# Performance work log

Hardware: AMD Instinct MI355X
Metric: run time of the kernel (lower is better)

The kernel has to match this reference:

```python
import jax, jax.numpy as jnp
import numpy as np

N, E = 50000, 800000
IN_DIM, HID, HEADS, OUT_DIM = 128, 64, 4, 40
NEG_SLOPE = 0.2


def setup_inputs() -> dict:
    key = jax.random.key(0)
    ks = jax.random.split(key, 12)
    x = jax.random.normal(ks[0], (N, IN_DIM), dtype=jnp.float32)
    edge_index = jax.random.randint(ks[1], (2, E), 0, N, dtype=jnp.int64)
    timesteps = jax.random.randint(ks[2], (N,), 0, 100, dtype=jnp.int64)
    s = 1.0 / np.sqrt(IN_DIM)
    W_proj = jax.random.uniform(ks[3], (IN_DIM, HID), jnp.float32, -s, s)
    b_proj = jnp.zeros((HID,), jnp.float32)
    time_emb = jax.random.normal(ks[4], (100, HID), dtype=jnp.float32)
    sg = 1.0 / np.sqrt(HID)
    W_gat = jax.random.uniform(ks[5], (HID, HEADS * HID), jnp.float32, -sg, sg)
    att_src = jax.random.uniform(ks[6], (HEADS, HID), jnp.float32, -sg, sg)
    att_dst = jax.random.uniform(ks[7], (HEADS, HID), jnp.float32, -sg, sg)
    b_gat = jnp.zeros((HEADS * HID,), jnp.float32)
    sc = 1.0 / np.sqrt(HEADS * HID)
    W_cls = jax.random.uniform(ks[8], (HEADS * HID, OUT_DIM), jnp.float32, -sc, sc)
    b_cls = jnp.zeros((OUT_DIM,), jnp.float32)
    return {"x": x, "edge_index": edge_index, "timesteps": timesteps,
            "W_proj": W_proj, "b_proj": b_proj, "time_emb": time_emb,
            "W_gat": W_gat, "att_src": att_src, "att_dst": att_dst, "b_gat": b_gat,
            "W_cls": W_cls, "b_cls": b_cls}


def reference(x, edge_index, timesteps, W_proj, b_proj, time_emb,
              W_gat, att_src, att_dst, b_gat, W_cls, b_cls):
    n = x.shape[0]
    # feature projection + ReLU + time embedding
    h0 = jax.nn.relu(x @ W_proj + b_proj) + time_emb[timesteps]  # [N, HID]
    # --- GATConv (PyG semantics, add_self_loops=True, concat heads) ---
    h = (h0 @ W_gat).reshape(n, HEADS, HID)              # [N, H, C]
    a_src = jnp.einsum('nhc,hc->nh', h, att_src)         # [N, H]
    a_dst = jnp.einsum('nhc,hc->nh', h, att_dst)
    loops = jnp.arange(n, dtype=edge_index.dtype)
    src = jnp.concatenate([edge_index[0], loops])        # [E+N]
    dst = jnp.concatenate([edge_index[1], loops])
    e = jax.nn.leaky_relu(a_src[src] + a_dst[dst], NEG_SLOPE)  # [E+N, H]
    # segment softmax over incoming edges per destination node
    m = jax.ops.segment_max(e, dst, num_segments=n)      # [N, H]
    p = jnp.exp(e - m[dst])
    denom = jax.ops.segment_sum(p, dst, num_segments=n)  # [N, H]
    alpha = p / (denom[dst] + 1e-16)                     # [E+N, H]
    msg = alpha[:, :, None] * h[src]                     # [E+N, H, C]
    agg = jax.ops.segment_sum(msg, dst, num_segments=n)  # [N, H, C]
    gat_out = agg.reshape(n, HEADS * HID) + b_gat
    # ReLU + (dropout is identity in eval) + classifier
    return jax.nn.relu(gat_out) @ W_cls + b_cls          # [N, OUT_DIM]
```

## Files before the change

### kernel.cpp

```cpp
#include <hip/hip_runtime.h>
#include <hip/hip_fp16.h>

#define IN_DIM 128
#define HID 64
#define HEADS 4
#define OUT_DIM 40
#define CAP 64
#define NEG 0.2f
#define PA_EPB 4096
#define BKT_SH 9
#define BKT_CAP 10240
#define GPAD 264

__device__ __forceinline__ float lrelu(float v) { return v > 0.f ? v : NEG * v; }

union HU { float2 f2; __half2 h2[2]; };
union HU2 { float4 f4; __half2 h2[4]; };

typedef _Float16 h2v __attribute__((ext_vector_type(2)));
union DU { float4 f4; h2v h[4]; };

typedef _Float16 f16x8 __attribute__((ext_vector_type(8)));
typedef float f32x4 __attribute__((ext_vector_type(4)));
union FU { float4 f4; f16x8 v; };

__device__ __forceinline__ float4 unpack_h4(float2 bits) {
    HU u; u.f2 = bits;
    float2 lo = __half22float2(u.h2[0]);
    float2 hi = __half22float2(u.h2[1]);
    return make_float4(lo.x, lo.y, hi.x, hi.y);
}

__global__ __launch_bounds__(256) void partA_kernel(
    const int* __restrict__ ei, int E, int nbkt, int paBlocks,
    int* __restrict__ cnt, unsigned int* __restrict__ ebuf,
    const float* __restrict__ Wg, const float* __restrict__ attS,
    const float* __restrict__ attD, const float* __restrict__ Wc,
    float* __restrict__ aSf, float* __restrict__ aDf,
    __half* __restrict__ WgT, __half* __restrict__ WcTg)
{
    if (blockIdx.x >= paBlocks) {
        int gid = (blockIdx.x - paBlocks) * 256 + threadIdx.x;
        if (gid < 256) {
            int k = gid >> 2, hd = gid & 3;
            const float* wr = Wg + k * 256 + hd * 64;
            const float* as = attS + hd * 64;
            const float* ad = attD + hd * 64;
            float ss = 0.f, dd = 0.f;
            for (int c = 0; c < 64; ++c) { float w = wr[c]; ss += w * as[c]; dd += w * ad[c]; }
            aSf[k * 4 + hd] = ss;
            aDf[k * 4 + hd] = dd;
        } else if (gid < 256 + 256 * HID) {
            int i = gid - 256;
            int o = i >> 6, k = i & 63;
            WgT[i] = __float2half(Wg[k * 256 + o]);
        } else if (gid < 256 + 256 * HID + OUT_DIM * 256) {
            int i = gid - 256 - 256 * HID;
            int o = i >> 8, k = i & 255;
            WcTg[i] = __float2half(Wc[k * OUT_DIM + o]);
        }
        return;
    }

    __shared__ int localCnt[128];
    __shared__ int baseArr[128];
    for (int i = threadIdx.x; i < nbkt; i += 256) localCnt[i] = 0;
    __syncthreads();

    const int e0 = blockIdx.x * PA_EPB + threadIdx.x;
    unsigned short l[16];
#pragma unroll
    for (int j = 0; j < 16; ++j) {
        int e = e0 + j * 256;
        if (e < E) {
            int d = ei[E + e];
            l[j] = (unsigned short)atomicAdd(&localCnt[d >> BKT_SH], 1);
        }
    }
    __syncthreads();
    for (int i = threadIdx.x; i < nbkt; i += 256)
        baseArr[i] = atomicAdd(&cnt[i], localCnt[i]);
    __syncthreads();
#pragma unroll
    for (int j = 0; j < 16; ++j) {
        int e = e0 + j * 256;
        if (e < E) {
            int s = ei[e];
            int d = ei[E + e];
            int b = d >> BKT_SH;
            int off = baseArr[b] + (int)l[j];
            if (off < BKT_CAP)
                ebuf[(size_t)b * BKT_CAP + off] =
                    ((unsigned)(d & ((1 << BKT_SH) - 1)) << 16) | (unsigned)s;
        }
    }
}

__global__ __launch_bounds__(256) void partBproj_kernel(
    const unsigned int* __restrict__ ebuf, const int* __restrict__ cnt,
    int* __restrict__ deg, unsigned short* __restrict__ csr, int nbkt,
    const float* __restrict__ x, const float* __restrict__ Wp,
    const float* __restrict__ bp, const float* __restrict__ temb,
    const int* __restrict__ ts, const float* __restrict__ aSf,
    const float* __restrict__ aDf,
    __half* __restrict__ h0h, float* __restrict__ aS, float* __restrict__ aD, int N)
{
    __shared__ __align__(16) char smem[IN_DIM * HID * 2];

    if ((int)blockIdx.x < nbkt) {
        int* cntL = (int*)smem;
        const int b = blockIdx.x;
        for (int i = threadIdx.x; i < 512; i += 256) cntL[i] = 0;
        __syncthreads();

        int cb = cnt[b]; cb = cb < BKT_CAP ? cb : BKT_CAP;
        const unsigned int* eb = ebuf + (size_t)b * BKT_CAP;
        const int d0 = b << BKT_SH;
        for (int i = threadIdx.x; i < cb; i += 256) {
            unsigned v = eb[i];
            int dloc = v >> 16;
            int slot = atomicAdd(&cntL[dloc], 1);
            if (slot < CAP)
                csr[((size_t)(d0 + dloc) << 6) + slot] = (unsigned short)(v & 0xFFFFu);
        }
        __syncthreads();
        for (int i = threadIdx.x; i < 512; i += 256) {
            int d = d0 + i;
            if (d < N) deg[d] = cntL[i];
        }
        return;
    }

    __half* Wl = (__half*)smem;
    for (int i = threadIdx.x * 8; i < IN_DIM * HID; i += 256 * 8) {
        float4 wa = *(const float4*)(Wp + i);
        float4 wb = *(const float4*)(Wp + i + 4);
        HU2 u;
        u.h2[0] = __floats2half2_rn(wa.x, wa.y);
        u.h2[1] = __floats2half2_rn(wa.z, wa.w);
        u.h2[2] = __floats2half2_rn(wb.x, wb.y);
        u.h2[3] = __floats2half2_rn(wb.z, wb.w);
        *(float4*)(Wl + i) = u.f4;
    }
    __syncthreads();

    const int t = threadIdx.x;
    const int lane = t & 63, wq = t >> 6;
    const int cg = lane & 15, ng = lane >> 4;
    const int c0 = cg * 4;
    const int nodeBase = ((int)blockIdx.x - nbkt) * 32 + wq * 8 + ng * 2;

    float4 acc[2];
#pragma unroll
    for (int j = 0; j < 2; ++j) acc[j] = make_float4(0.f, 0.f, 0.f, 0.f);

    for (int k0 = 0; k0 < IN_DIM; k0 += 4) {
        float4 xv[2];
#pragma unroll
        for (int j = 0; j < 2; ++j) {
            int n = nodeBase + j; n = n < N ? n : N - 1;
            xv[j] = *(const float4*)(x + (size_t)n * IN_DIM + k0);
        }
        float4 wv[4];
#pragma unroll
        for (int kk = 0; kk < 4; ++kk)
            wv[kk] = unpack_h4(*(const float2*)(Wl + (k0 + kk) * HID + c0));
#pragma unroll
        for (int j = 0; j < 2; ++j) {
            const float* xs = (const float*)&xv[j];
#pragma unroll
            for (int kk = 0; kk < 4; ++kk) {
                acc[j].x += xs[kk] * wv[kk].x;
                acc[j].y += xs[kk] * wv[kk].y;
                acc[j].z += xs[kk] * wv[kk].z;
                acc[j].w += xs[kk] * wv[kk].w;
            }
        }
    }
    const float4 bb = *(const float4*)(bp + c0);
    float4 s0 = *(const float4*)(aSf + (c0 + 0) * 4);
    float4 s1 = *(const float4*)(aSf + (c0 + 1) * 4);
    float4 s2 = *(const float4*)(aSf + (c0 + 2) * 4);
    float4 s3 = *(const float4*)(aSf + (c0 + 3) * 4);
    float4 d0 = *(const float4*)(aDf + (c0 + 0) * 4);
    float4 d1 = *(const float4*)(aDf + (c0 + 1) * 4);
    float4 d2 = *(const float4*)(aDf + (c0 + 2) * 4);
    float4 d3 = *(const float4*)(aDf + (c0 + 3) * 4);
#pragma unroll
    for (int j = 0; j < 2; ++j) {
        int n = nodeBase + j;
        float4 r = make_float4(0.f, 0.f, 0.f, 0.f);
        if (n < N) {
            int tv = ts[n];
            float4 te = *(const float4*)(temb + (size_t)tv * HID + c0);
            r.x = fmaxf(acc[j].x + bb.x, 0.f) + te.x;
            r.y = fmaxf(acc[j].y + bb.y, 0.f) + te.y;
            r.z = fmaxf(acc[j].z + bb.z, 0.f) + te.z;
            r.w = fmaxf(acc[j].w + bb.w, 0.f) + te.w;
            HU u;
            u.h2[0] = __floats2half2_rn(r.x, r.y);
            u.h2[1] = __floats2half2_rn(r.z, r.w);
            *(float2*)(h0h + (size_t)n * HID + c0) = u.f2;
        }
        float4 pS, pD;
        pS.x = r.x * s0.x + r.y * s1.x + r.z * s2.x + r.w * s3.x;
        pS.y = r.x * s0.y + r.y * s1.y + r.z * s2.y + r.w * s3.y;
        pS.z = r.x * s0.z + r.y * s1.z + r.z * s2.z + r.w * s3.z;
        pS.w = r.x * s0.w + r.y * s1.w + r.z * s2.w + r.w * s3.w;
        pD.x = r.x * d0.x + r.y * d1.x + r.z * d2.x + r.w * d3.x;
        pD.y = r.x * d0.y + r.y * d1.y + r.z * d2.y + r.w * d3.y;
        pD.z = r.x * d0.z + r.y * d1.z + r.z * d2.z + r.w * d3.z;
        pD.w = r.x * d0.w + r.y * d1.w + r.z * d2.w + r.w * d3.w;
#pragma unroll
        for (int off = 8; off > 0; off >>= 1) {
            pS.x += __shfl_down(pS.x, off); pS.y += __shfl_down(pS.y, off);
            pS.z += __shfl_down(pS.z, off); pS.w += __shfl_down(pS.w, off);
            pD.x += __shfl_down(pD.x, off); pD.y += __shfl_down(pD.y, off);
            pD.z += __shfl_down(pD.z, off); pD.w += __shfl_down(pD.w, off);
        }
        if (cg == 0 && n < N) {
            *(float4*)(aS + (size_t)n * 4) = pS;
            *(float4*)(aD + (size_t)n * 4) = pD;
        }
    }
}

__global__ __launch_bounds__(256) void agg_kernel(
    const __half* __restrict__ h0h, const float* __restrict__ aS,
    const float* __restrict__ aD, const int* __restrict__ deg,
    const unsigned short* __restrict__ csr, __half* __restrict__ agg0h, int N)
{
    __shared__ float p_lds[4 * CAP * HEADS];
    __shared__ int   s_lds[4 * CAP];

    const int t = threadIdx.x;
    const int lane = t & 63, wq = t >> 6;
    const int n = blockIdx.x * 4 + wq;
    if (n >= N) return;
    const int hd16 = lane >> 4, li = lane & 15;

    const float adn = aD[n * 4 + hd16];
    const float es = lrelu(aS[n * 4 + hd16] + adn);

    int dn = deg[n]; dn = dn < CAP ? dn : CAP;
    const unsigned short* cs = csr + (size_t)n * CAP;
    float* pL = p_lds + wq * CAP * HEADS;
    int*   sL = s_lds + wq * CAP;

    float m = -1e30f;
    for (int i = li; i < dn; i += 16) {
        int src = cs[i];
        if (hd16 == 0) sL[i] = src << 7;
        float e = lrelu(aS[src * 4 + hd16] + adn);
        pL[i * HEADS + hd16] = e;
        m = fmaxf(m, e);
    }
#pragma unroll
    for (int off = 8; off > 0; off >>= 1)
        m = fmaxf(m, __shfl_xor(m, off));
    m = fmaxf(m, es);
    float mh[4], esh[4];
#pragma unroll
    for (int h = 0; h < 4; ++h) {
        mh[h]  = __shfl(m, h * 16);
        esh[h] = __shfl(es, h * 16);
    }

    float sp = 0.f;
    for (int idx = lane; idx < dn * 4; idx += 64) {
        float p = __expf(pL[idx] - mh[idx & 3]);
        pL[idx] = p;
        sp += p;
    }
#pragma unroll
    for (int off = 4; off < 64; off <<= 1)
        sp += __shfl_xor(sp, off);
    float pselfh[4], invh[4];
#pragma unroll
    for (int h = 0; h < 4; ++h) {
        float sh = __shfl(sp, h);
        pselfh[h] = __expf(esh[h] - mh[h]);
        invh[h] = 1.f / (sh + pselfh[h] + 1e-16f);
    }

    const int half = lane >> 5;
    const int ch2 = lane & 31;
    const char* hb = (const char*)h0h;
    const int laneByte = ch2 << 2;

    float2 acc[4];
    {
        float lo = 0.f, hi = 0.f;
        if (half == 0) {
            __half2 v2 = *(const __half2*)(hb + ((size_t)n << 7) + laneByte);
            float2 f = __half22float2(v2);
            lo = f.x; hi = f.y;
        }
#pragma unroll
        for (int h = 0; h < 4; ++h) {
            acc[h].x = pselfh[h] * lo;
            acc[h].y = pselfh[h] * hi;
        }
    }
    int i = 0;
    for (; i + 8 <= dn; i += 8) {
        int off0 = sL[i + 0 + half];
        int off1 = sL[i + 2 + half];
        int off2 = sL[i + 4 + half];
        int off3 = sL[i + 6 + half];
        __half2 v0 = *(const __half2*)(hb + off0 + laneByte);
        __half2 v1 = *(const __half2*)(hb + off1 + laneByte);
        __half2 v2 = *(const __half2*)(hb + off2 + laneByte);
        __half2 v3 = *(const __half2*)(hb + off3 + laneByte);
        float4 p0 = *(const float4*)(pL + (i + 0 + half) * 4);
        float4 p1 = *(const float4*)(pL + (i + 2 + half) * 4);
        float4 p2 = *(const float4*)(pL + (i + 4 + half) * 4);
        float4 p3 = *(const float4*)(pL + (i + 6 + half) * 4);
        float2 f;
        f = __half22float2(v0);
        acc[0].x += p0.x * f.x; acc[0].y += p0.x * f.y;
        acc[1].x += p0.y * f.x; acc[1].y += p0.y * f.y;
        acc[2].x += p0.z * f.x; acc[2].y += p0.z * f.y;
        acc[3].x += p0.w * f.x; acc[3].y += p0.w * f.y;
        f = __half22float2(v1);
        acc[0].x += p1.x * f.x; acc[0].y += p1.x * f.y;
        acc[1].x += p1.y * f.x; acc[1].y += p1.y * f.y;
        acc[2].x += p1.z * f.x; acc[2].y += p1.z * f.y;
        acc[3].x += p1.w * f.x; acc[3].y += p1.w * f.y;
        f = __half22float2(v2);
        acc[0].x += p2.x * f.x; acc[0].y += p2.x * f.y;
        acc[1].x += p2.y * f.x; acc[1].y += p2.y * f.y;
        acc[2].x += p2.z * f.x; acc[2].y += p2.z * f.y;
        acc[3].x += p2.w * f.x; acc[3].y += p2.w * f.y;
        f = __half22float2(v3);
        acc[0].x += p3.x * f.x; acc[0].y += p3.x * f.y;
        acc[1].x += p3.y * f.x; acc[1].y += p3.y * f.y;
        acc[2].x += p3.z * f.x; acc[2].y += p3.z * f.y;
        acc[3].x += p3.w * f.x; acc[3].y += p3.w * f.y;
    }
    for (; i + 2 <= dn; i += 2) {
        int off0 = sL[i + half];
        __half2 v0 = *(const __half2*)(hb + off0 + laneByte);
        float4 p0 = *(const float4*)(pL + (i + half) * 4);
        float2 f = __half22float2(v0);
        acc[0].x += p0.x * f.x; acc[0].y += p0.x * f.y;
        acc[1].x += p0.y * f.x; acc[1].y += p0.y * f.y;
        acc[2].x += p0.z * f.x; acc[2].y += p0.z * f.y;
        acc[3].x += p0.w * f.x; acc[3].y += p0.w * f.y;
    }
    if (i < dn && half == 0) {
        int off0 = sL[i];
        __half2 v0 = *(const __half2*)(hb + off0 + laneByte);
        float4 p0 = *(const float4*)(pL + i * 4);
        float2 f = __half22float2(v0);
        acc[0].x += p0.x * f.x; acc[0].y += p0.x * f.y;
        acc[1].x += p0.y * f.x; acc[1].y += p0.y * f.y;
        acc[2].x += p0.z * f.x; acc[2].y += p0.z * f.y;
        acc[3].x += p0.w * f.x; acc[3].y += p0.w * f.y;
    }
#pragma unroll
    for (int h = 0; h < 4; ++h) {
        acc[h].x += __shfl_xor(acc[h].x, 32);
        acc[h].y += __shfl_xor(acc[h].y, 32);
    }
    if (lane < 32) {
        __half2* dst = (__half2*)(agg0h + (size_t)n * 256);
#pragma unroll
        for (int h = 0; h < 4; ++h)
            dst[h * 32 + ch2] = __floats2half2_rn(acc[h].x * invh[h],
                                                  acc[h].y * invh[h]);
    }
}

__global__ __launch_bounds__(256) void gatcls_kernel(
    const __half* __restrict__ agg0h, const __half* __restrict__ WgT,
    const float* __restrict__ bg, const __half* __restrict__ WcTg,
    const float* __restrict__ bc, float* __restrict__ out, int N)
{
    __shared__ __half gtile[32 * GPAD];

    const int t = threadIdx.x;
    const int lane = t & 63, wq = t >> 6;
    const int m16 = lane & 15, quad = lane >> 4;
    const int nodeBase = blockIdx.x * 32;

    {
        const int h = wq;
        f32x4 acc[2][4];
#pragma unroll
        for (int mt = 0; mt < 2; ++mt)
#pragma unroll
            for (int nt = 0; nt < 4; ++nt)
                acc[mt][nt] = (f32x4){0.f, 0.f, 0.f, 0.f};

#pragma unroll
        for (int ks = 0; ks < 2; ++ks) {
            FU a[2], b[4];
#pragma unroll
            for (int mt = 0; mt < 2; ++mt) {
                int n = nodeBase + mt * 16 + m16; n = n < N ? n : N - 1;
                a[mt].f4 = *(const float4*)(agg0h + (size_t)n * 256 + h * 64 + ks * 32 + quad * 8);
            }
#pragma unroll
            for (int nt = 0; nt < 4; ++nt) {
                int o = h * 64 + nt * 16 + m16;
                b[nt].f4 = *(const float4*)(WgT + o * 64 + ks * 32 + quad * 8);
            }
#pragma unroll
            for (int mt = 0; mt < 2; ++mt)
#pragma unroll
                for (int nt = 0; nt < 4; ++nt)
                    acc[mt][nt] = __builtin_amdgcn_mfma_f32_16x16x32_f16(
                        a[mt].v, b[nt].v, acc[mt][nt], 0, 0, 0);
        }
#pragma unroll
        for (int nt = 0; nt < 4; ++nt) {
            int o = h * 64 + nt * 16 + m16;
            float bv = bg[o];
#pragma unroll
            for (int mt = 0; mt < 2; ++mt) {
#pragma unroll
                for (int r = 0; r < 4; ++r) {
                    int nloc = mt * 16 + quad * 4 + r;
                    gtile[nloc * GPAD + o] = __float2half(fmaxf(acc[mt][nt][r] + bv, 0.f));
                }
            }
        }
    }
    __syncthreads();

    {
        const int mt = wq >> 1;
        const int ntCount = (wq & 1) ? 1 : 2;
        const int ntBase = (wq & 1) ? 2 : 0;
        f32x4 acc2[2];
        acc2[0] = (f32x4){0.f, 0.f, 0.f, 0.f};
        acc2[1] = (f32x4){0.f, 0.f, 0.f, 0.f};
#pragma unroll
        for (int ks = 0; ks < 8; ++ks) {
            FU a; a.f4 = *(const float4*)(gtile + (mt * 16 + m16) * GPAD + ks * 32 + quad * 8);
            for (int q = 0; q < ntCount; ++q) {
                int o = (ntBase + q) * 16 + m16;
                int oc = o < OUT_DIM ? o : OUT_DIM - 1;
                FU b; b.f4 = *(const float4*)(WcTg + oc * 256 + ks * 32 + quad * 8);
                acc2[q] = __builtin_amdgcn_mfma_f32_16x16x32_f16(a.v, b.v, acc2[q], 0, 0, 0);
            }
        }
        for (int q = 0; q < ntCount; ++q) {
            int o = (ntBase + q) * 16 + m16;
            if (o < OUT_DIM) {
                float bv = bc[o];
#pragma unroll
                for (int r = 0; r < 4; ++r) {
                    int n = nodeBase + mt * 16 + quad * 4 + r;
                    if (n < N) out[(size_t)n * OUT_DIM + o] = acc2[q][r] + bv;
                }
            }
        }
    }
}

extern "C" void kernel_launch(void* const* d_in, const int* in_sizes, int n_in,
                              void* d_out, int out_size, void* d_ws, size_t ws_size,
                              hipStream_t stream) {
    const float* x    = (const float*)d_in[0];
    const int*   ei   = (const int*)d_in[1];
    const int*   ts   = (const int*)d_in[2];
    const float* Wp   = (const float*)d_in[3];
    const float* bp   = (const float*)d_in[4];
    const float* temb = (const float*)d_in[5];
    const float* Wg   = (const float*)d_in[6];
    const float* attS = (const float*)d_in[7];
    const float* attD = (const float*)d_in[8];
    const float* bg   = (const float*)d_in[9];
    const float* Wc   = (const float*)d_in[10];
    const float* bc   = (const float*)d_in[11];
    float* out = (float*)d_out;

    const int N = in_sizes[0] / IN_DIM;
    const int E = in_sizes[1] / 2;
    const int nbkt = (N + (1 << BKT_SH) - 1) >> BKT_SH;

    char* w = (char*)d_ws;
    __half*         h0h   = (__half*)w;         w += (size_t)N * HID * 2;
    __half*         agg0h = (__half*)w;         w += (size_t)N * 256 * 2;
    float*          aS    = (float*)w;          w += (size_t)N * HEADS * 4;
    float*          aD    = (float*)w;          w += (size_t)N * HEADS * 4;
    int*            deg   = (int*)w;            w += (size_t)N * 4;
    unsigned short* csr   = (unsigned short*)w; w += (size_t)N * CAP * 2;
    unsigned int*   ebuf  = (unsigned int*)w;   w += (size_t)nbkt * BKT_CAP * 4;
    int*            cnt   = (int*)w;            w += (size_t)nbkt * 4;
    float*          aSf   = (float*)w;          w += 256 * 4;
    float*          aDf   = (float*)w;          w += 256 * 4;
    __half*         WgT   = (__half*)w;         w += (size_t)256 * HID * 2;
    __half*         WcTg  = (__half*)w;         w += (size_t)OUT_DIM * 256 * 2;

    const int paBlocks = (E + PA_EPB - 1) / PA_EPB;
    const int prepWork = 256 + 256 * HID + OUT_DIM * 256;
    const int prepBlocks = (prepWork + 255) / 256;
    const int projBlocks = (N + 31) / 32;

    hipMemsetAsync(cnt, 0, (size_t)nbkt * 4, stream);
    partA_kernel<<<paBlocks + prepBlocks, 256, 0, stream>>>(
        ei, E, nbkt, paBlocks, cnt, ebuf, Wg, attS, attD, Wc, aSf, aDf, WgT, WcTg);
    partBproj_kernel<<<nbkt + projBlocks, 256, 0, stream>>>(
        ebuf, cnt, deg, csr, nbkt, x, Wp, bp, temb, ts, aSf, aDf, h0h, aS, aD, N);
    agg_kernel<<<(N + 3) / 4, 256, 0, stream>>>(h0h, aS, aD, deg, csr, agg0h, N);
    gatcls_kernel<<<(N + 31) / 32, 256, 0, stream>>>(agg0h, WgT, bg, WcTg, bc, out, N);
}
```

Before: 199.1 us.

## Fuse attention aggregation with GAT projection and classifier kernel

Merges the aggregation kernel and the GAT-projection/classifier kernel into one. Each block handles 32 nodes, with each wave aggregating 8 nodes in sequence into a shared-memory fp16 tile that then feeds the MFMA stages directly. This removes the global agg0h round trip (N×256 halves written and read back) and one kernel launch. In exchange, each block has fewer resident waves working on the latency-bound gather, more LDS use, and extra barriers.

```diff
diff --git a/kernel.cpp b/kernel.cpp
--- a/kernel.cpp
+++ b/kernel.cpp
@@ -16,9 +16,6 @@
 
 union HU { float2 f2; __half2 h2[2]; };
 union HU2 { float4 f4; __half2 h2[4]; };
-
-typedef _Float16 h2v __attribute__((ext_vector_type(2)));
-union DU { float4 f4; h2v h[4]; };
 
 typedef _Float16 f16x8 __attribute__((ext_vector_type(8)));
 typedef float f32x4 __attribute__((ext_vector_type(4)));
@@ -225,165 +222,165 @@
     }
 }
 
-__global__ __launch_bounds__(256) void agg_kernel(
+__global__ __launch_bounds__(256) void aggcls_kernel(
     const __half* __restrict__ h0h, const float* __restrict__ aS,
     const float* __restrict__ aD, const int* __restrict__ deg,
-    const unsigned short* __restrict__ csr, __half* __restrict__ agg0h, int N)
+    const unsigned short* __restrict__ csr,
+    const __half* __restrict__ WgT, const float* __restrict__ bg,
+    const __half* __restrict__ WcTg, const float* __restrict__ bc,
+    float* __restrict__ out, int N)
 {
-    __shared__ float p_lds[4 * CAP * HEADS];
-    __shared__ int   s_lds[4 * CAP];
+    __shared__ __half aggL[32 * GPAD];
+    __shared__ union {
+        struct { float p[4 * CAP * HEADS]; int s[4 * CAP]; } g;
+        __half gtile[32 * GPAD];
+    } su;
 
     const int t = threadIdx.x;
     const int lane = t & 63, wq = t >> 6;
-    const int n = blockIdx.x * 4 + wq;
-    if (n >= N) return;
+    const int nodeBase = blockIdx.x * 32;
     const int hd16 = lane >> 4, li = lane & 15;
-
-    const float adn = aD[n * 4 + hd16];
-    const float es = lrelu(aS[n * 4 + hd16] + adn);
-
-    int dn = deg[n]; dn = dn < CAP ? dn : CAP;
-    const unsigned short* cs = csr + (size_t)n * CAP;
-    float* pL = p_lds + wq * CAP * HEADS;
-    int*   sL = s_lds + wq * CAP;
-
-    float m = -1e30f;
-    for (int i = li; i < dn; i += 16) {
-        int src = cs[i];
-        if (hd16 == 0) sL[i] = src << 7;
-        float e = lrelu(aS[src * 4 + hd16] + adn);
-        pL[i * HEADS + hd16] = e;
-        m = fmaxf(m, e);
-    }
-#pragma unroll
-    for (int off = 8; off > 0; off >>= 1)
-        m = fmaxf(m, __shfl_xor(m, off));
-    m = fmaxf(m, es);
-    float mh[4], esh[4];
-#pragma unroll
-    for (int h = 0; h < 4; ++h) {
-        mh[h]  = __shfl(m, h * 16);
-        esh[h] = __shfl(es, h * 16);
-    }
-
-    float sp = 0.f;
-    for (int idx = lane; idx < dn * 4; idx += 64) {
-        float p = __expf(pL[idx] - mh[idx & 3]);
-        pL[idx] = p;
-        sp += p;
-    }
-#pragma unroll
-    for (int off = 4; off < 64; off <<= 1)
-        sp += __shfl_xor(sp, off);
-    float pselfh[4], invh[4];
-#pragma unroll
-    for (int h = 0; h < 4; ++h) {
-        float sh = __shfl(sp, h);
-        pselfh[h] = __expf(esh[h] - mh[h]);
-        invh[h] = 1.f / (sh + pselfh[h] + 1e-16f);
-    }
-
     const int half = lane >> 5;
     const int ch2 = lane & 31;
     const char* hb = (const char*)h0h;
     const int laneByte = ch2 << 2;
 
-    float2 acc[4];
-    {
-        float lo = 0.f, hi = 0.f;
-        if (half == 0) {
-            __half2 v2 = *(const __half2*)(hb + ((size_t)n << 7) + laneByte);
-            float2 f = __half22float2(v2);
-            lo = f.x; hi = f.y;
-        }
+    float* pL = su.g.p + wq * CAP * HEADS;
+    int*   sL = su.g.s + wq * CAP;
+
+    for (int j = 0; j < 8; ++j) {
+        const int nloc = wq * 8 + j;
+        const int n = nodeBase + nloc;
+        if (n >= N) break;
+
+        const float adn = aD[n * 4 + hd16];
+        const float es = lrelu(aS[n * 4 + hd16] + adn);
+
+        int dn = deg[n]; dn = dn < CAP ? dn : CAP;
+        const unsigned short* cs = csr + (size_t)n * CAP;
+
+        float m = -1e30f;
+        for (int i = li; i < dn; i += 16) {
+            int src = cs[i];
+            if (hd16 == 0) sL[i] = src << 7;
+            float e = lrelu(aS[src * 4 + hd16] + adn);
+            pL[i * HEADS + hd16] = e;
+            m = fmaxf(m, e);
+        }
+#pragma unroll
+        for (int off = 8; off > 0; off >>= 1)
+            m = fmaxf(m, __shfl_xor(m, off));
+        m = fmaxf(m, es);
+        float mh[4], esh[4];
 #pragma unroll
         for (int h = 0; h < 4; ++h) {
-            acc[h].x = pselfh[h] * lo;
-            acc[h].y = pselfh[h] * hi;
-        }
-    }
-    int i = 0;
-    for (; i + 8 <= dn; i += 8) {
-        int off0 = sL[i + 0 + half];
-        int off1 = sL[i + 2 + half];
-        int off2 = sL[i + 4 + half];
-        int off3 = sL[i + 6 + half];
-        __half2 v0 = *(const __half2*)(hb + off0 + laneByte);
-        __half2 v1 = *(const __half2*)(hb + off1 + laneByte);
-        __half2 v2 = *(const __half2*)(hb + off2 + laneByte);
-        __half2 v3 = *(const __half2*)(hb + off3 + laneByte);
-        float4 p0 = *(const float4*)(pL + (i + 0 + half) * 4);
-        float4 p1 = *(const float4*)(pL + (i + 2 + half) * 4);
-        float4 p2 = *(const float4*)(pL + (i + 4 + half) * 4);
-        float4 p3 = *(const float4*)(pL + (i + 6 + half) * 4);
-        float2 f;
-        f = __half22float2(v0);
-        acc[0].x += p0.x * f.x; acc[0].y += p0.x * f.y;
-        acc[1].x += p0.y * f.x; acc[1].y += p0.y * f.y;
-        acc[2].x += p0.z * f.x; acc[2].y += p0.z * f.y;
-        acc[3].x += p0.w * f.x; acc[3].y += p0.w * f.y;
-        f = __half22float2(v1);
-        acc[0].x += p1.x * f.x; acc[0].y += p1.x * f.y;
-        acc[1].x += p1.y * f.x; acc[1].y += p1.y * f.y;
-        acc[2].x += p1.z * f.x; acc[2].y += p1.z * f.y;
-        acc[3].x += p1.w * f.x; acc[3].y += p1.w * f.y;
-        f = __half22float2(v2);
-        acc[0].x += p2.x * f.x; acc[0].y += p2.x * f.y;
-        acc[1].x += p2.y * f.x; acc[1].y += p2.y * f.y;
-        acc[2].x += p2.z * f.x; acc[2].y += p2.z * f.y;
-        acc[3].x += p2.w * f.x; acc[3].y += p2.w * f.y;
-        f = __half22float2(v3);
-        acc[0].x += p3.x * f.x; acc[0].y += p3.x * f.y;
-        acc[1].x += p3.y * f.x; acc[1].y += p3.y * f.y;
-        acc[2].x += p3.z * f.x; acc[2].y += p3.z * f.y;
-        acc[3].x += p3.w * f.x; acc[3].y += p3.w * f.y;
-    }
-    for (; i + 2 <= dn; i += 2) {
-        int off0 = sL[i + half];
-        __half2 v0 = *(const __half2*)(hb + off0 + laneByte);
-        float4 p0 = *(const float4*)(pL + (i + half) * 4);
-        float2 f = __half22float2(v0);
-        acc[0].x += p0.x * f.x; acc[0].y += p0.x * f.y;
-        acc[1].x += p0.y * f.x; acc[1].y += p0.y * f.y;
-        acc[2].x += p0.z * f.x; acc[2].y += p0.z * f.y;
-        acc[3].x += p0.w * f.x; acc[3].y += p0.w * f.y;
-    }
-    if (i < dn && half == 0) {
-        int off0 = sL[i];
-        __half2 v0 = *(const __half2*)(hb + off0 + laneByte);
-        float4 p0 = *(const float4*)(pL + i * 4);
-        float2 f = __half22float2(v0);
-        acc[0].x += p0.x * f.x; acc[0].y += p0.x * f.y;
-        acc[1].x += p0.y * f.x; acc[1].y += p0.y * f.y;
-        acc[2].x += p0.z * f.x; acc[2].y += p0.z * f.y;
-        acc[3].x += p0.w * f.x; acc[3].y += p0.w * f.y;
-    }
-#pragma unroll
-    for (int h = 0; h < 4; ++h) {
-        acc[h].x += __shfl_xor(acc[h].x, 32);
-        acc[h].y += __shfl_xor(acc[h].y, 32);
-    }
-    if (lane < 32) {
-        __half2* dst = (__half2*)(agg0h + (size_t)n * 256);
-#pragma unroll
-        for (int h = 0; h < 4; ++h)
-            dst[h * 32 + ch2] = __floats2half2_rn(acc[h].x * invh[h],
-                                                  acc[h].y * invh[h]);
-    }
-}
-
-__global__ __launch_bounds__(256) void gatcls_kernel(
-    const __half* __restrict__ agg0h, const __half* __restrict__ WgT,
-    const float* __restrict__ bg, const __half* __restrict__ WcTg,
-    const float* __restrict__ bc, float* __restrict__ out, int N)
-{
-    __shared__ __half gtile[32 * GPAD];
-
-    const int t = threadIdx.x;
-    const int lane = t & 63, wq = t >> 6;
+            mh[h]  = __shfl(m, h * 16);
+            esh[h] = __shfl(es, h * 16);
+        }
+
+        float sp = 0.f;
+        for (int idx = lane; idx < dn * 4; idx += 64) {
+            float p = __expf(pL[idx] - mh[idx & 3]);
+            pL[idx] = p;
+            sp += p;
+        }
+#pragma unroll
+        for (int off = 4; off < 64; off <<= 1)
+            sp += __shfl_xor(sp, off);
+        float pselfh[4], invh[4];
+#pragma unroll
+        for (int h = 0; h < 4; ++h) {
+            float sh = __shfl(sp, h);
+            pselfh[h] = __expf(esh[h] - mh[h]);
+            invh[h] = 1.f / (sh + pselfh[h] + 1e-16f);
+        }
+
+        float2 acc[4];
+        {
+            float lo = 0.f, hi = 0.f;
+            if (half == 0) {
+                __half2 v2 = *(const __half2*)(hb + ((size_t)n << 7) + laneByte);
+                float2 f = __half22float2(v2);
+                lo = f.x; hi = f.y;
+            }
+#pragma unroll
+            for (int h = 0; h < 4; ++h) {
+                acc[h].x = pselfh[h] * lo;
+                acc[h].y = pselfh[h] * hi;
+            }
+        }
+        int i = 0;
+        for (; i + 8 <= dn; i += 8) {
+            int off0 = sL[i + 0 + half];
+            int off1 = sL[i + 2 + half];
+            int off2 = sL[i + 4 + half];
+            int off3 = sL[i + 6 + half];
+            __half2 v0 = *(const __half2*)(hb + off0 + laneByte);
+            __half2 v1 = *(const __half2*)(hb + off1 + laneByte);
+            __half2 v2 = *(const __half2*)(hb + off2 + laneByte);
+            __half2 v3 = *(const __half2*)(hb + off3 + laneByte);
+            float4 p0 = *(const float4*)(pL + (i + 0 + half) * 4);
+            float4 p1 = *(const float4*)(pL + (i + 2 + half) * 4);
+            float4 p2 = *(const float4*)(pL + (i + 4 + half) * 4);
+            float4 p3 = *(const float4*)(pL + (i + 6 + half) * 4);
+            float2 f;
+            f = __half22float2(v0);
+            acc[0].x += p0.x * f.x; acc[0].y += p0.x * f.y;
+            acc[1].x += p0.y * f.x; acc[1].y += p0.y * f.y;
+            acc[2].x += p0.z * f.x; acc[2].y += p0.z * f.y;
+            acc[3].x += p0.w * f.x; acc[3].y += p0.w * f.y;
+            f = __half22float2(v1);
+            acc[0].x += p1.x * f.x; acc[0].y += p1.x * f.y;
+            acc[1].x += p1.y * f.x; acc[1].y += p1.y * f.y;
+            acc[2].x += p1.z * f.x; acc[2].y += p1.z * f.y;
+            acc[3].x += p1.w * f.x; acc[3].y += p1.w * f.y;
+            f = __half22float2(v2);
+            acc[0].x += p2.x * f.x; acc[0].y += p2.x * f.y;
+            acc[1].x += p2.y * f.x; acc[1].y += p2.y * f.y;
+            acc[2].x += p2.z * f.x; acc[2].y += p2.z * f.y;
+            acc[3].x += p2.w * f.x; acc[3].y += p2.w * f.y;
+            f = __half22float2(v3);
+            acc[0].x += p3.x * f.x; acc[0].y += p3.x * f.y;
+            acc[1].x += p3.y * f.x; acc[1].y += p3.y * f.y;
+            acc[2].x += p3.z * f.x; acc[2].y += p3.z * f.y;
+            acc[3].x += p3.w * f.x; acc[3].y += p3.w * f.y;
+        }
+        for (; i + 2 <= dn; i += 2) {
+            int off0 = sL[i + half];
+            __half2 v0 = *(const __half2*)(hb + off0 + laneByte);
+            float4 p0 = *(const float4*)(pL + (i + half) * 4);
+            float2 f = __half22float2(v0);
+            acc[0].x += p0.x * f.x; acc[0].y += p0.x * f.y;
+            acc[1].x += p0.y * f.x; acc[1].y += p0.y * f.y;
+            acc[2].x += p0.z * f.x; acc[2].y += p0.z * f.y;
+            acc[3].x += p0.w * f.x; acc[3].y += p0.w * f.y;
+        }
+        if (i < dn && half == 0) {
+            int off0 = sL[i];
+            __half2 v0 = *(const __half2*)(hb + off0 + laneByte);
+            float4 p0 = *(const float4*)(pL + i * 4);
+            float2 f = __half22float2(v0);
+            acc[0].x += p0.x * f.x; acc[0].y += p0.x * f.y;
+            acc[1].x += p0.y * f.x; acc[1].y += p0.y * f.y;
+            acc[2].x += p0.z * f.x; acc[2].y += p0.z * f.y;
+            acc[3].x += p0.w * f.x; acc[3].y += p0.w * f.y;
+        }
+#pragma unroll
+        for (int h = 0; h < 4; ++h) {
+            acc[h].x += __shfl_xor(acc[h].x, 32);
+            acc[h].y += __shfl_xor(acc[h].y, 32);
+        }
+        if (lane < 32) {
+            __half2* dst = (__half2*)(aggL + nloc * GPAD);
+#pragma unroll
+            for (int h = 0; h < 4; ++h)
+                dst[h * 32 + ch2] = __floats2half2_rn(acc[h].x * invh[h],
+                                                      acc[h].y * invh[h]);
+        }
+    }
+    __syncthreads();
+
     const int m16 = lane & 15, quad = lane >> 4;
-    const int nodeBase = blockIdx.x * 32;
-
     {
         const int h = wq;
         f32x4 acc[2][4];
@@ -397,10 +394,8 @@
         for (int ks = 0; ks < 2; ++ks) {
             FU a[2], b[4];
 #pragma unroll
-            for (int mt = 0; mt < 2; ++mt) {
-                int n = nodeBase + mt * 16 + m16; n = n < N ? n : N - 1;
-                a[mt].f4 = *(const float4*)(agg0h + (size_t)n * 256 + h * 64 + ks * 32 + quad * 8);
-            }
+            for (int mt = 0; mt < 2; ++mt)
+                a[mt].f4 = *(const float4*)(aggL + (mt * 16 + m16) * GPAD + h * 64 + ks * 32 + quad * 8);
 #pragma unroll
             for (int nt = 0; nt < 4; ++nt) {
                 int o = h * 64 + nt * 16 + m16;
@@ -413,6 +408,7 @@
                     acc[mt][nt] = __builtin_amdgcn_mfma_f32_16x16x32_f16(
                         a[mt].v, b[nt].v, acc[mt][nt], 0, 0, 0);
         }
+        __syncthreads();
 #pragma unroll
         for (int nt = 0; nt < 4; ++nt) {
             int o = h * 64 + nt * 16 + m16;
@@ -422,7 +418,7 @@
 #pragma unroll
                 for (int r = 0; r < 4; ++r) {
                     int nloc = mt * 16 + quad * 4 + r;
-                    gtile[nloc * GPAD + o] = __float2half(fmaxf(acc[mt][nt][r] + bv, 0.f));
+                    su.gtile[nloc * GPAD + o] = __float2half(fmaxf(acc[mt][nt][r] + bv, 0.f));
                 }
             }
         }
@@ -438,7 +434,7 @@
         acc2[1] = (f32x4){0.f, 0.f, 0.f, 0.f};
 #pragma unroll
         for (int ks = 0; ks < 8; ++ks) {
-            FU a; a.f4 = *(const float4*)(gtile + (mt * 16 + m16) * GPAD + ks * 32 + quad * 8);
+            FU a; a.f4 = *(const float4*)(su.gtile + (mt * 16 + m16) * GPAD + ks * 32 + quad * 8);
             for (int q = 0; q < ntCount; ++q) {
                 int o = (ntBase + q) * 16 + m16;
                 int oc = o < OUT_DIM ? o : OUT_DIM - 1;
@@ -483,7 +479,6 @@
 
     char* w = (char*)d_ws;
     __half*         h0h   = (__half*)w;         w += (size_t)N * HID * 2;
-    __half*         agg0h = (__half*)w;         w += (size_t)N * 256 * 2;
     float*          aS    = (float*)w;          w += (size_t)N * HEADS * 4;
     float*          aD    = (float*)w;          w += (size_t)N * HEADS * 4;
     int*            deg   = (int*)w;            w += (size_t)N * 4;
@@ -505,6 +500,6 @@
         ei, E, nbkt, paBlocks, cnt, ebuf, Wg, attS, attD, Wc, aSf, aDf, WgT, WcTg);
     partBproj_kernel<<<nbkt + projBlocks, 256, 0, stream>>>(
         ebuf, cnt, deg, csr, nbkt, x, Wp, bp, temb, ts, aSf, aDf, h0h, aS, aD, N);
-    agg_kernel<<<(N + 3) / 4, 256, 0, stream>>>(h0h, aS, aD, deg, csr, agg0h, N);
-    gatcls_kernel<<<(N + 31) / 32, 256, 0, stream>>>(agg0h, WgT, bg, WcTg, bc, out, N);
+    aggcls_kernel<<<(N + 31) / 32, 256, 0, stream>>>(
+        h0h, aS, aD, deg, csr, WgT, bg, WcTg, bc, out, N);
 }
```

Result: slower. 220.0 us (+10.5%).

## Use MFMA for input projection and attention-score GEMMs in partBproj

Applied to the files above, without the earlier changes.

Replaces the scalar FMA projection x@W_proj with f16 MFMA 16x16x32 instructions using a transposed fp16 W_proj prepared in the prep blocks. h0 is staged in padded LDS, then a second small MFMA against a precomputed W_gat·att matrix produces aS/aD, replacing the shuffle reductions. This drops the per-block conversion of W_proj into LDS, but rounds x to fp16 before the multiply, which adds precision error.

```diff
diff --git a/kernel.cpp b/kernel.cpp
--- a/kernel.cpp
+++ b/kernel.cpp
@@ -11,33 +11,26 @@
 #define BKT_SH 9
 #define BKT_CAP 10240
 #define GPAD 264
+#define HGP 72
 
 __device__ __forceinline__ float lrelu(float v) { return v > 0.f ? v : NEG * v; }
 
 union HU { float2 f2; __half2 h2[2]; };
 union HU2 { float4 f4; __half2 h2[4]; };
-
-typedef _Float16 h2v __attribute__((ext_vector_type(2)));
-union DU { float4 f4; h2v h[4]; };
 
 typedef _Float16 f16x8 __attribute__((ext_vector_type(8)));
 typedef float f32x4 __attribute__((ext_vector_type(4)));
 union FU { float4 f4; f16x8 v; };
-
-__device__ __forceinline__ float4 unpack_h4(float2 bits) {
-    HU u; u.f2 = bits;
-    float2 lo = __half22float2(u.h2[0]);
-    float2 hi = __half22float2(u.h2[1]);
-    return make_float4(lo.x, lo.y, hi.x, hi.y);
-}
 
 __global__ __launch_bounds__(256) void partA_kernel(
     const int* __restrict__ ei, int E, int nbkt, int paBlocks,
     int* __restrict__ cnt, unsigned int* __restrict__ ebuf,
     const float* __restrict__ Wg, const float* __restrict__ attS,
     const float* __restrict__ attD, const float* __restrict__ Wc,
+    const float* __restrict__ Wp,
     float* __restrict__ aSf, float* __restrict__ aDf,
-    __half* __restrict__ WgT, __half* __restrict__ WcTg)
+    __half* __restrict__ WgT, __half* __restrict__ WcTg,
+    __half* __restrict__ WpT, __half* __restrict__ BsdT)
 {
     if (blockIdx.x >= paBlocks) {
         int gid = (blockIdx.x - paBlocks) * 256 + threadIdx.x;
@@ -58,6 +51,21 @@
             int i = gid - 256 - 256 * HID;
             int o = i >> 8, k = i & 255;
             WcTg[i] = __float2half(Wc[k * OUT_DIM + o]);
+        } else if (gid < 26880 + HID * IN_DIM) {
+            int i = gid - 26880;
+            int o = i >> 7, k = i & 127;
+            WpT[i] = __float2half(Wp[k * HID + o]);
+        } else if (gid < 26880 + HID * IN_DIM + 16 * HID) {
+            int i = gid - 26880 - HID * IN_DIM;
+            int n2 = i >> 6, k = i & 63;
+            float v = 0.f;
+            if (n2 < 8) {
+                int hd = n2 & 3;
+                const float* wr = Wg + k * 256 + hd * 64;
+                const float* av = (n2 < 4) ? (attS + hd * 64) : (attD + hd * 64);
+                for (int c = 0; c < 64; ++c) v += wr[c] * av[c];
+            }
+            BsdT[i] = __float2half(v);
         }
         return;
     }
@@ -99,13 +107,12 @@
 __global__ __launch_bounds__(256) void partBproj_kernel(
     const unsigned int* __restrict__ ebuf, const int* __restrict__ cnt,
     int* __restrict__ deg, unsigned short* __restrict__ csr, int nbkt,
-    const float* __restrict__ x, const float* __restrict__ Wp,
+    const float* __restrict__ x, const __half* __restrict__ WpT,
     const float* __restrict__ bp, const float* __restrict__ temb,
-    const int* __restrict__ ts, const float* __restrict__ aSf,
-    const float* __restrict__ aDf,
+    const int* __restrict__ ts, const __half* __restrict__ BsdT,
     __half* __restrict__ h0h, float* __restrict__ aS, float* __restrict__ aD, int N)
 {
-    __shared__ __align__(16) char smem[IN_DIM * HID * 2];
+    __shared__ __align__(16) char smem[32 * HGP * 2];
 
     if ((int)blockIdx.x < nbkt) {
         int* cntL = (int*)smem;
@@ -131,96 +138,84 @@
         return;
     }
 
-    __half* Wl = (__half*)smem;
-    for (int i = threadIdx.x * 8; i < IN_DIM * HID; i += 256 * 8) {
-        float4 wa = *(const float4*)(Wp + i);
-        float4 wb = *(const float4*)(Wp + i + 4);
-        HU2 u;
-        u.h2[0] = __floats2half2_rn(wa.x, wa.y);
-        u.h2[1] = __floats2half2_rn(wa.z, wa.w);
-        u.h2[2] = __floats2half2_rn(wb.x, wb.y);
-        u.h2[3] = __floats2half2_rn(wb.z, wb.w);
-        *(float4*)(Wl + i) = u.f4;
-    }
-    __syncthreads();
-
+    __half* h0L = (__half*)smem;
     const int t = threadIdx.x;
     const int lane = t & 63, wq = t >> 6;
-    const int cg = lane & 15, ng = lane >> 4;
-    const int c0 = cg * 4;
-    const int nodeBase = ((int)blockIdx.x - nbkt) * 32 + wq * 8 + ng * 2;
-
-    float4 acc[2];
-#pragma unroll
-    for (int j = 0; j < 2; ++j) acc[j] = make_float4(0.f, 0.f, 0.f, 0.f);
-
-    for (int k0 = 0; k0 < IN_DIM; k0 += 4) {
-        float4 xv[2];
-#pragma unroll
-        for (int j = 0; j < 2; ++j) {
-            int n = nodeBase + j; n = n < N ? n : N - 1;
-            xv[j] = *(const float4*)(x + (size_t)n * IN_DIM + k0);
-        }
-        float4 wv[4];
-#pragma unroll
-        for (int kk = 0; kk < 4; ++kk)
-            wv[kk] = unpack_h4(*(const float2*)(Wl + (k0 + kk) * HID + c0));
-#pragma unroll
-        for (int j = 0; j < 2; ++j) {
-            const float* xs = (const float*)&xv[j];
-#pragma unroll
-            for (int kk = 0; kk < 4; ++kk) {
-                acc[j].x += xs[kk] * wv[kk].x;
-                acc[j].y += xs[kk] * wv[kk].y;
-                acc[j].z += xs[kk] * wv[kk].z;
-                acc[j].w += xs[kk] * wv[kk].w;
-            }
-        }
-    }
-    const float4 bb = *(const float4*)(bp + c0);
-    float4 s0 = *(const float4*)(aSf + (c0 + 0) * 4);
-    float4 s1 = *(const float4*)(aSf + (c0 + 1) * 4);
-    float4 s2 = *(const float4*)(aSf + (c0 + 2) * 4);
-    float4 s3 = *(const float4*)(aSf + (c0 + 3) * 4);
-    float4 d0 = *(const float4*)(aDf + (c0 + 0) * 4);
-    float4 d1 = *(const float4*)(aDf + (c0 + 1) * 4);
-    float4 d2 = *(const float4*)(aDf + (c0 + 2) * 4);
-    float4 d3 = *(const float4*)(aDf + (c0 + 3) * 4);
-#pragma unroll
-    for (int j = 0; j < 2; ++j) {
-        int n = nodeBase + j;
-        float4 r = make_float4(0.f, 0.f, 0.f, 0.f);
-        if (n < N) {
-            int tv = ts[n];
-            float4 te = *(const float4*)(temb + (size_t)tv * HID + c0);
-            r.x = fmaxf(acc[j].x + bb.x, 0.f) + te.x;
-            r.y = fmaxf(acc[j].y + bb.y, 0.f) + te.y;
-            r.z = fmaxf(acc[j].z + bb.z, 0.f) + te.z;
-            r.w = fmaxf(acc[j].w + bb.w, 0.f) + te.w;
-            HU u;
-            u.h2[0] = __floats2half2_rn(r.x, r.y);
-            u.h2[1] = __floats2half2_rn(r.z, r.w);
-            *(float2*)(h0h + (size_t)n * HID + c0) = u.f2;
-        }
-        float4 pS, pD;
-        pS.x = r.x * s0.x + r.y * s1.x + r.z * s2.x + r.w * s3.x;
-        pS.y = r.x * s0.y + r.y * s1.y + r.z * s2.y + r.w * s3.y;
-        pS.z = r.x * s0.z + r.y * s1.z + r.z * s2.z + r.w * s3.z;
-        pS.w = r.x * s0.w + r.y * s1.w + r.z * s2.w + r.w * s3.w;
-        pD.x = r.x * d0.x + r.y * d1.x + r.z * d2.x + r.w * d3.x;
-        pD.y = r.x * d0.y + r.y * d1.y + r.z * d2.y + r.w * d3.y;
-        pD.z = r.x * d0.z + r.y * d1.z + r.z * d2.z + r.w * d3.z;
-        pD.w = r.x * d0.w + r.y * d1.w + r.z * d2.w + r.w * d3.w;
-#pragma unroll
-        for (int off = 8; off > 0; off >>= 1) {
-            pS.x += __shfl_down(pS.x, off); pS.y += __shfl_down(pS.y, off);
-            pS.z += __shfl_down(pS.z, off); pS.w += __shfl_down(pS.w, off);
-            pD.x += __shfl_down(pD.x, off); pD.y += __shfl_down(pD.y, off);
-            pD.z += __shfl_down(pD.z, off); pD.w += __shfl_down(pD.w, off);
-        }
-        if (cg == 0 && n < N) {
-            *(float4*)(aS + (size_t)n * 4) = pS;
-            *(float4*)(aD + (size_t)n * 4) = pD;
+    const int m16 = lane & 15, quad = lane >> 4;
+    const int mt = wq >> 1;
+    const int ntb = (wq & 1) * 2;
+    const int nodeBase = ((int)blockIdx.x - nbkt) * 32;
+
+    f32x4 acc[2];
+    acc[0] = (f32x4){0.f, 0.f, 0.f, 0.f};
+    acc[1] = (f32x4){0.f, 0.f, 0.f, 0.f};
+
+    {
+        int n = nodeBase + mt * 16 + m16; n = n < N ? n : N - 1;
+        const float* xr = x + (size_t)n * IN_DIM;
+#pragma unroll
+        for (int ks = 0; ks < 4; ++ks) {
+            float4 xa = *(const float4*)(xr + ks * 32 + quad * 8);
+            float4 xb = *(const float4*)(xr + ks * 32 + quad * 8 + 4);
+            HU2 u;
+            u.h2[0] = __floats2half2_rn(xa.x, xa.y);
+            u.h2[1] = __floats2half2_rn(xa.z, xa.w);
+            u.h2[2] = __floats2half2_rn(xb.x, xb.y);
+            u.h2[3] = __floats2half2_rn(xb.z, xb.w);
+            FU a; a.f4 = u.f4;
+#pragma unroll
+            for (int q = 0; q < 2; ++q) {
+                int o = (ntb + q) * 16 + m16;
+                FU b; b.f4 = *(const float4*)(WpT + o * IN_DIM + ks * 32 + quad * 8);
+                acc[q] = __builtin_amdgcn_mfma_f32_16x16x32_f16(a.v, b.v, acc[q], 0, 0, 0);
+            }
+        }
+    }
+
+    {
+        float bv[2];
+#pragma unroll
+        for (int q = 0; q < 2; ++q) bv[q] = bp[(ntb + q) * 16 + m16];
+#pragma unroll
+        for (int r = 0; r < 4; ++r) {
+            int nloc = mt * 16 + quad * 4 + r;
+            int n = nodeBase + nloc;
+            if (n < N) {
+                int tv = ts[n];
+                const float* te = temb + (size_t)tv * HID;
+#pragma unroll
+                for (int q = 0; q < 2; ++q) {
+                    int c = (ntb + q) * 16 + m16;
+                    float v = fmaxf(acc[q][r] + bv[q], 0.f) + te[c];
+                    h0L[nloc * HGP + c] = __float2half(v);
+                }
+            }
+        }
+    }
+    __syncthreads();
+
+    {
+        int row = t >> 3, ch = (t & 7) * 8;
+        int n = nodeBase + row;
+        if (n < N)
+            *(float4*)(h0h + (size_t)n * HID + ch) = *(const float4*)(h0L + row * HGP + ch);
+    }
+
+    if (wq < 2) {
+        f32x4 acc2 = (f32x4){0.f, 0.f, 0.f, 0.f};
+#pragma unroll
+        for (int ks = 0; ks < 2; ++ks) {
+            FU a; a.f4 = *(const float4*)(h0L + (wq * 16 + m16) * HGP + ks * 32 + quad * 8);
+            FU b; b.f4 = *(const float4*)(BsdT + m16 * 64 + ks * 32 + quad * 8);
+            acc2 = __builtin_amdgcn_mfma_f32_16x16x32_f16(a.v, b.v, acc2, 0, 0, 0);
+        }
+#pragma unroll
+        for (int r = 0; r < 4; ++r) {
+            int n = nodeBase + wq * 16 + quad * 4 + r;
+            if (n < N) {
+                if (m16 < 4)      aS[n * 4 + m16]       = acc2[r];
+                else if (m16 < 8) aD[n * 4 + (m16 - 4)] = acc2[r];
+            }
         }
     }
 }
@@ -494,17 +489,21 @@
     float*          aDf   = (float*)w;          w += 256 * 4;
     __half*         WgT   = (__half*)w;         w += (size_t)256 * HID * 2;
     __half*         WcTg  = (__half*)w;         w += (size_t)OUT_DIM * 256 * 2;
+    __half*         WpT   = (__half*)w;         w += (size_t)HID * IN_DIM * 2;
+    __half*         BsdT  = (__half*)w;         w += (size_t)16 * HID * 2;
 
     const int paBlocks = (E + PA_EPB - 1) / PA_EPB;
-    const int prepWork = 256 + 256 * HID + OUT_DIM * 256;
+    const int prepWork = 256 + 256 * HID + OUT_DIM * 256
+                       + HID * IN_DIM + 16 * HID;
     const int prepBlocks = (prepWork + 255) / 256;
     const int projBlocks = (N + 31) / 32;
 
     hipMemsetAsync(cnt, 0, (size_t)nbkt * 4, stream);
     partA_kernel<<<paBlocks + prepBlocks, 256, 0, stream>>>(
-        ei, E, nbkt, paBlocks, cnt, ebuf, Wg, attS, attD, Wc, aSf, aDf, WgT, WcTg);
+        ei, E, nbkt, paBlocks, cnt, ebuf, Wg, attS, attD, Wc, Wp,
+        aSf, aDf, WgT, WcTg, WpT, BsdT);
     partBproj_kernel<<<nbkt + projBlocks, 256, 0, stream>>>(
-        ebuf, cnt, deg, csr, nbkt, x, Wp, bp, temb, ts, aSf, aDf, h0h, aS, aD, N);
+        ebuf, cnt, deg, csr, nbkt, x, WpT, bp, temb, ts, BsdT, h0h, aS, aD, N);
     agg_kernel<<<(N + 3) / 4, 256, 0, stream>>>(h0h, aS, aD, deg, csr, agg0h, N);
     gatcls_kernel<<<(N + 31) / 32, 256, 0, stream>>>(agg0h, WgT, bg, WcTg, bc, out, N);
 }
```

New measurement: 198.6 us, median of 2. About the same (-0.2%).
